# Optimization experiments

Measured on AMD Instinct MI355X. Metric: run time of the kernel, lower is better.

Reference implementation:

```python
import jax, jax.numpy as jnp
import numpy as np

N = 50000      # nodes
E = 800000     # edges
IN = 128       # in_channels
HID = 64       # hidden_channels (per head)
HEADS = 2      # GAT heads
OUT = 64       # out_channels (classes)


def segment_softmax(e, seg, num_segments):
    # softmax of per-edge scores grouped by destination node
    m = jax.ops.segment_max(e, seg, num_segments=num_segments)
    ex = jnp.exp(e - m[seg])
    s = jax.ops.segment_sum(ex, seg, num_segments=num_segments)
    return ex / s[seg]


def setup_inputs() -> dict:
    key = jax.random.key(0)
    ks = jax.random.split(key, 12)
    sc = 0.05
    return {
        "x": jax.random.normal(ks[0], (N, IN), dtype=jnp.float32),
        "edge_index": jax.random.randint(ks[1], (2, E), 0, N),
        # GATConv params: lin (no bias), att_src/att_dst, output bias
        "W1": jax.random.normal(ks[2], (IN, HEADS * HID), dtype=jnp.float32) * sc,
        "att_src": jax.random.normal(ks[3], (HEADS, HID), dtype=jnp.float32) * sc,
        "att_dst": jax.random.normal(ks[4], (HEADS, HID), dtype=jnp.float32) * sc,
        "b1": jnp.zeros((HEADS * HID,), dtype=jnp.float32),
        # TransformerConv params (heads=1): q/k/v linears + skip linear
        "Wq": jax.random.normal(ks[5], (HEADS * HID, OUT), dtype=jnp.float32) * sc,
        "bq": jnp.zeros((OUT,), dtype=jnp.float32),
        "Wk": jax.random.normal(ks[6], (HEADS * HID, OUT), dtype=jnp.float32) * sc,
        "bk": jnp.zeros((OUT,), dtype=jnp.float32),
        "Wv": jax.random.normal(ks[7], (HEADS * HID, OUT), dtype=jnp.float32) * sc,
        "bv": jnp.zeros((OUT,), dtype=jnp.float32),
        "Wskip": jax.random.normal(ks[8], (HEADS * HID, OUT), dtype=jnp.float32) * sc,
        "bskip": jnp.zeros((OUT,), dtype=jnp.float32),
    }


def reference(x, edge_index, W1, att_src, att_dst, b1,
              Wq, bq, Wk, bk, Wv, bv, Wskip, bskip):
    n = x.shape[0]
    # ---- GATConv (concat=True, add_self_loops=True, negative_slope=0.2) ----
    loops = jnp.arange(n)
    src = jnp.concatenate([edge_index[0], loops])  # message source j
    dst = jnp.concatenate([edge_index[1], loops])  # message target i
    h = (x @ W1).reshape(n, HEADS, HID)            # [N,H,C]
    a_src = (h * att_src).sum(-1)                  # [N,H]
    a_dst = (h * att_dst).sum(-1)                  # [N,H]
    e = jax.nn.leaky_relu(a_src[src] + a_dst[dst], 0.2)   # [E+N,H]
    alpha = segment_softmax(e, dst, n)                     # [E+N,H]
    out1 = jax.ops.segment_sum(alpha[..., None] * h[src], dst, num_segments=n)
    x1 = jax.nn.relu(out1.reshape(n, HEADS * HID) + b1)    # [N,H*C]
    # ---- TransformerConv (heads=1, root_weight=True, no self-loops) ----
    q = x1 @ Wq + bq
    k = x1 @ Wk + bk
    v = x1 @ Wv + bv
    s2, d2 = edge_index[0], edge_index[1]
    scores = (q[d2] * k[s2]).sum(-1) / jnp.sqrt(jnp.float32(OUT))  # [E]
    al = segment_softmax(scores, d2, n)
    agg = jax.ops.segment_sum(al[:, None] * v[s2], d2, num_segments=n)
    out = agg + x1 @ Wskip + bskip
    return jax.nn.log_softmax(out, axis=1)
```

## Files before the change

kernel.cpp:

```cpp
#include <hip/hip_runtime.h>
#include <math.h>

typedef unsigned short u16;
typedef unsigned int u32;
typedef unsigned char u8;

using bf16x8 = __attribute__((ext_vector_type(8))) short;
using f32x4  = __attribute__((ext_vector_type(4))) float;
typedef __attribute__((ext_vector_type(2))) float vf2;

__device__ __forceinline__ float lrelu02(float x){ return x > 0.f ? x : 0.2f * x; }

__device__ __forceinline__ float bf2f(u16 u){
  union { u32 i; float f; } v; v.i = ((u32)u) << 16; return v.f;
}
__device__ __forceinline__ u16 f2bf(float f){
  union { float ff; u32 i; } v; v.ff = f;
  u32 x = v.i;
  return (u16)((x + 0x7fffu + ((x >> 16) & 1u)) >> 16);
}
__device__ __forceinline__ u32 pack2(float lo, float hi){
  return (u32)f2bf(lo) | ((u32)f2bf(hi) << 16);
}
__device__ __forceinline__ u8 f2fp8(float v){
  return (u8)(__builtin_amdgcn_cvt_pk_fp8_f32(v, v, 0, false) & 0xff);
}
__device__ __forceinline__ vf2 fma2(vf2 a, vf2 b, vf2 c){
  return __builtin_elementwise_fma(a, b, c);
}

__global__ __launch_bounds__(256) void cast_x_kernel(const float* __restrict__ x,
                                                     u16* __restrict__ xbf, int total8){
  int i = blockIdx.x * 256 + threadIdx.x;
  if (i >= total8) return;
  const float4* x4 = (const float4*)x;
  float4 a = x4[(size_t)i * 2];
  float4 b = x4[(size_t)i * 2 + 1];
  uint4 w;
  w.x = pack2(a.x, a.y);
  w.y = pack2(a.z, a.w);
  w.z = pack2(b.x, b.y);
  w.w = pack2(b.z, b.w);
  ((uint4*)xbf)[i] = w;
}

__global__ __launch_bounds__(256) void cast_h_kernel(const u16* __restrict__ h2,
                                                     u8* __restrict__ h8, int total16){
  int i = blockIdx.x * 256 + threadIdx.x;
  if (i >= total16) return;
  const uint4* hp = (const uint4*)(h2 + (size_t)i * 16);
  uint4 a = hp[0], b = hp[1];
  u32 w0 = 0, w1 = 0, w2 = 0, w3 = 0;
  w0 = __builtin_amdgcn_cvt_pk_fp8_f32(bf2f((u16)(a.x & 0xffffu)), bf2f((u16)(a.x >> 16)), w0, false);
  w0 = __builtin_amdgcn_cvt_pk_fp8_f32(bf2f((u16)(a.y & 0xffffu)), bf2f((u16)(a.y >> 16)), w0, true);
  w1 = __builtin_amdgcn_cvt_pk_fp8_f32(bf2f((u16)(a.z & 0xffffu)), bf2f((u16)(a.z >> 16)), w1, false);
  w1 = __builtin_amdgcn_cvt_pk_fp8_f32(bf2f((u16)(a.w & 0xffffu)), bf2f((u16)(a.w >> 16)), w1, true);
  w2 = __builtin_amdgcn_cvt_pk_fp8_f32(bf2f((u16)(b.x & 0xffffu)), bf2f((u16)(b.x >> 16)), w2, false);
  w2 = __builtin_amdgcn_cvt_pk_fp8_f32(bf2f((u16)(b.y & 0xffffu)), bf2f((u16)(b.y >> 16)), w2, true);
  w3 = __builtin_amdgcn_cvt_pk_fp8_f32(bf2f((u16)(b.z & 0xffffu)), bf2f((u16)(b.z >> 16)), w3, false);
  w3 = __builtin_amdgcn_cvt_pk_fp8_f32(bf2f((u16)(b.w & 0xffffu)), bf2f((u16)(b.w >> 16)), w3, true);
  uint4 o = {w0, w1, w2, w3};
  ((uint4*)h8)[i] = o;
}

__global__ __launch_bounds__(256) void prep_w_kernel(const float* __restrict__ W1,
                                                     const float* __restrict__ Wq,
                                                     const float* __restrict__ Wk,
                                                     const float* __restrict__ Wv,
                                                     const float* __restrict__ Ws,
                                                     const float* __restrict__ att_src,
                                                     const float* __restrict__ att_dst,
                                                     u16* __restrict__ w1t,
                                                     u16* __restrict__ wt2,
                                                     u16* __restrict__ wxt){
  int idx = blockIdx.x * 256 + threadIdx.x;
  if (idx < 16384){
    int j = idx >> 7, k = idx & 127;
    w1t[j * 128 + k] = f2bf(W1[k * 128 + j]);
  } else if (idx < 49152){
    int i = idx - 16384;
    int mat = i >> 13;
    int r = i & 8191;
    int j = r >> 7, k = r & 127;
    const float* W = (mat == 0) ? Wq : (mat == 1) ? Wk : (mat == 2) ? Wv : Ws;
    wt2[(mat * 64 + j) * 128 + k] = f2bf(W[k * 64 + j]);
  } else if (idx < 49664){
    int i = idx - 49152;
    int j = i >> 7, k = i & 127;
    const float* av = (j & 2) ? att_dst : att_src;
    int head = j & 1;
    float s = 0.f;
#pragma unroll 8
    for (int c = 0; c < 64; c++) s += W1[k * 128 + head * 64 + c] * av[head * 64 + c];
    wxt[j * 128 + k] = f2bf(s);
  } else if (idx < 51200){
    int i = idx - 49664;
    wxt[512 + i] = 0;
  }
}

__global__ __launch_bounds__(256) void gemm1_mfma(const u16* __restrict__ xbf,
                                                  const u16* __restrict__ w1t,
                                                  const u16* __restrict__ wxt,
                                                  u16* __restrict__ h2,
                                                  float* __restrict__ asrc,
                                                  float* __restrict__ adst, int n){
  int wid = threadIdx.x >> 6, lane = threadIdx.x & 63;
  int rl = lane & 15, kh = lane >> 4;
  int br = blockIdx.x * 64 + wid * 16;
  int arow = br + rl; if (arow > n - 1) arow = n - 1;
  const u16* abase = xbf + (size_t)arow * 128 + kh * 8;
  f32x4 acc[9];
#pragma unroll
  for (int t = 0; t < 9; t++) acc[t] = (f32x4){0.f, 0.f, 0.f, 0.f};
#pragma unroll
  for (int ks = 0; ks < 4; ks++){
    bf16x8 a = *(const bf16x8*)(abase + ks * 32);
#pragma unroll
    for (int t = 0; t < 8; t++){
      bf16x8 b = *(const bf16x8*)(w1t + (size_t)(t * 16 + rl) * 128 + ks * 32 + kh * 8);
      acc[t] = __builtin_amdgcn_mfma_f32_16x16x32_bf16(a, b, acc[t], 0, 0, 0);
    }
    bf16x8 bx = *(const bf16x8*)(wxt + (size_t)rl * 128 + ks * 32 + kh * 8);
    acc[8] = __builtin_amdgcn_mfma_f32_16x16x32_bf16(a, bx, acc[8], 0, 0, 0);
  }
  int orow0 = br + kh * 4;
#pragma unroll
  for (int r = 0; r < 4; r++){
    int orow = orow0 + r;
    if (orow < n){
      u16* hp = h2 + (size_t)orow * 128 + rl;
#pragma unroll
      for (int t = 0; t < 8; t++) hp[t * 16] = f2bf(acc[t][r]);
      if (rl < 4){
        float vlv = acc[8][r];
        if (rl < 2) asrc[orow * 2 + rl] = vlv;
        else        adst[orow * 2 + (rl - 2)] = vlv;
      }
    }
  }
}

__global__ __launch_bounds__(256) void gemm2_mfma(const u16* __restrict__ x1bf,
                                                  const u16* __restrict__ wt2,
                                                  const float* __restrict__ bq,
                                                  const float* __restrict__ bk,
                                                  const float* __restrict__ bv,
                                                  const float* __restrict__ bs,
                                                  float* __restrict__ q,
                                                  u8* __restrict__ kv8,
                                                  float* __restrict__ skip, int n){
  int wid = threadIdx.x >> 6, lane = threadIdx.x & 63;
  int rl = lane & 15, kh = lane >> 4;
  int br = blockIdx.x * 64 + wid * 16;
  int arow = br + rl; if (arow > n - 1) arow = n - 1;
  const u16* abase = x1bf + (size_t)arow * 128 + kh * 8;
  f32x4 acc[16];
#pragma unroll
  for (int t = 0; t < 16; t++) acc[t] = (f32x4){0.f, 0.f, 0.f, 0.f};
#pragma unroll
  for (int ks = 0; ks < 4; ks++){
    bf16x8 a = *(const bf16x8*)(abase + ks * 32);
#pragma unroll
    for (int t = 0; t < 16; t++){
      bf16x8 b = *(const bf16x8*)(wt2 + (size_t)(t * 16 + rl) * 128 + ks * 32 + kh * 8);
      acc[t] = __builtin_amdgcn_mfma_f32_16x16x32_bf16(a, b, acc[t], 0, 0, 0);
    }
  }
  float bias_t[16];
#pragma unroll
  for (int t = 0; t < 16; t++){
    const float* bb = (t < 4) ? bq : (t < 8) ? bk : (t < 12) ? bv : bs;
    bias_t[t] = bb[(t & 3) * 16 + rl];
  }
  int orow0 = br + kh * 4;
#pragma unroll
  for (int r = 0; r < 4; r++){
    int orow = orow0 + r;
    if (orow >= n) continue;
#pragma unroll
    for (int t = 0; t < 16; t++){
      int c = (t & 3) * 16 + rl;
      float val = acc[t][r] + bias_t[t];
      if (t < 4)       q[(size_t)orow * 64 + c]    = val;
      else if (t < 8)  kv8[(size_t)orow * 128 + (c >> 3) * 16 + (c & 7)]     = f2fp8(val);
      else if (t < 12) kv8[(size_t)orow * 128 + (c >> 3) * 16 + 8 + (c & 7)] = f2fp8(val);
      else             skip[(size_t)orow * 64 + c] = val;
    }
  }
}

__global__ __launch_bounds__(256) void bucket_hist_kernel(const int* __restrict__ dst,
                                                          int* __restrict__ bc, int E){
  __shared__ int h[512];
  for (int i = threadIdx.x; i < 512; i += 256) h[i] = 0;
  __syncthreads();
  int base = blockIdx.x * 4096;
#pragma unroll
  for (int i = 0; i < 16; i++){
    int e = base + i * 256 + threadIdx.x;
    if (e < E) atomicAdd(&h[dst[e] >> 7], 1);
  }
  __syncthreads();
  for (int i = threadIdx.x; i < 512; i += 256)
    if (h[i]) atomicAdd(&bc[i], h[i]);
}

__global__ __launch_bounds__(256) void bucket_scan_kernel(const int* __restrict__ bc,
                                                          int* __restrict__ bbase,
                                                          int* __restrict__ bcur){
  __shared__ int tmp[5];
  int tid = threadIdx.x;
  int c0 = bc[2 * tid], c1 = bc[2 * tid + 1];
  int s = c0 + c1, incl = s;
  int lane = tid & 63, wid = tid >> 6;
#pragma unroll
  for (int o = 1; o < 64; o <<= 1){
    int t = __shfl_up(incl, o);
    if (lane >= o) incl += t;
  }
  if (lane == 63) tmp[wid] = incl;
  __syncthreads();
  if (tid == 0){
    int run = 0;
#pragma unroll
    for (int w2 = 0; w2 < 4; w2++){ int t = tmp[w2]; tmp[w2] = run; run += t; }
    tmp[4] = run;
  }
  __syncthreads();
  int excl = tmp[wid] + incl - s;
  bbase[2 * tid]     = excl;      bbase[2 * tid + 1] = excl + c0;
  bcur[2 * tid]      = excl;      bcur[2 * tid + 1]  = excl + c0;
  if (tid == 255) bbase[512] = tmp[4];
}

__global__ __launch_bounds__(256) void multisplit_kernel(const int* __restrict__ src,
                                                         const int* __restrict__ dst,
                                                         int* __restrict__ bcur,
                                                         uint2* __restrict__ ebuf, int E){
  __shared__ int h[512];
  __shared__ int gb[512];
  __shared__ int cur[512];
  int tid = threadIdx.x;
  for (int i = tid; i < 512; i += 256){ h[i] = 0; cur[i] = 0; }
  __syncthreads();
  int base = blockIdx.x * 4096;
  int myd[16];
#pragma unroll
  for (int i = 0; i < 16; i++){
    int e = base + i * 256 + tid;
    myd[i] = (e < E) ? dst[e] : -1;
    if (myd[i] >= 0) atomicAdd(&h[myd[i] >> 7], 1);
  }
  __syncthreads();
  for (int i = tid; i < 512; i += 256){
    int c = h[i];
    gb[i] = c ? atomicAdd(&bcur[i], c) : 0;
  }
  __syncthreads();
#pragma unroll
  for (int i = 0; i < 16; i++){
    if (myd[i] >= 0){
      int e = base + i * 256 + tid;
      int b = myd[i] >> 7;
      int r = atomicAdd(&cur[b], 1);
      uint2 ed; ed.x = (u32)src[e]; ed.y = (u32)myd[i];
      ebuf[gb[b] + r] = ed;
    }
  }
}

__global__ __launch_bounds__(256) void bucket_csr_kernel(const uint2* __restrict__ ebuf,
                                                         const int* __restrict__ bbase,
                                                         int* __restrict__ offsets,
                                                         int* __restrict__ csr,
                                                         int n, int E, int nb){
  __shared__ int deg[128];
  __shared__ int loff[128];
  __shared__ int cur[128];
  int b = blockIdx.x, tid = threadIdx.x;
  int base = bbase[b], end = bbase[b + 1];
  if (tid < 128) deg[tid] = 0;
  __syncthreads();
  for (int e = base + tid; e < end; e += 256)
    atomicAdd(&deg[ebuf[e].y & 127], 1);
  __syncthreads();
  if (tid < 64){
    int v0 = deg[2 * tid], v1 = deg[2 * tid + 1];
    int s = v0 + v1, incl = s;
#pragma unroll
    for (int o = 1; o < 64; o <<= 1){
      int t = __shfl_up(incl, o);
      if (tid >= o) incl += t;
    }
    int excl = incl - s;
    loff[2 * tid] = excl; loff[2 * tid + 1] = excl + v0;
  }
  __syncthreads();
  int node0 = b << 7;
  if (tid < 128){
    cur[tid] = loff[tid];
    int node = node0 + tid;
    if (node < n) offsets[node] = base + loff[tid];
  }
  if (b == nb - 1 && tid == 0) offsets[n] = E;
  __syncthreads();
  for (int e = base + tid; e < end; e += 256){
    uint2 ed = ebuf[e];
    int r = atomicAdd(&cur[ed.y & 127], 1);
    csr[base + r] = (int)ed.x;
  }
}

__global__ __launch_bounds__(256) void gat_agg_kernel(const u8* __restrict__ h8,
                                                      const float* __restrict__ asrc,
                                                      const float* __restrict__ adst,
                                                      const int* __restrict__ off,
                                                      const int* __restrict__ csr_src,
                                                      const float* __restrict__ b1,
                                                      u16* __restrict__ x1bf, int n){
  int node = blockIdx.x * 4 + (threadIdx.x >> 6);
  int lane = threadIdx.x & 63;
  if (node >= n) return;
  int s0 = off[node];
  int d  = off[node + 1] - s0;
  int g = lane >> 3;
  int sub = lane & 7;
  int chb = sub * 16;
  int head = sub >> 2;
  float2 ad  = ((const float2*)adst)[node];
  float2 asl = ((const float2*)asrc)[node];
  float ad_own = head ? ad.y : ad.x;
  float pself = __expf(lrelu02((head ? asl.y : asl.x) + ad_own));
  vf2 acc[8];
#pragma unroll
  for (int i = 0; i < 8; i++) acc[i] = (vf2){0.f, 0.f};
  float ps = 0.f;
#pragma unroll 2
  for (int base = 0; base < d; base += 8){
    int idx = base + g;
    bool valid = idx < d;
    int sj = csr_src[s0 + (valid ? idx : d - 1)];
    float2 as = ((const float2*)asrc)[sj];
    float p = valid ? __expf(lrelu02((head ? as.y : as.x) + ad_own)) : 0.f;
    ps += p;
    uint4 w = *(const uint4*)(h8 + (size_t)sj * 128 + chb);
    vf2 p2 = {p, p};
    acc[0] = fma2(p2, __builtin_amdgcn_cvt_pk_f32_fp8((int)w.x, false), acc[0]);
    acc[1] = fma2(p2, __builtin_amdgcn_cvt_pk_f32_fp8((int)w.x, true),  acc[1]);
    acc[2] = fma2(p2, __builtin_amdgcn_cvt_pk_f32_fp8((int)w.y, false), acc[2]);
    acc[3] = fma2(p2, __builtin_amdgcn_cvt_pk_f32_fp8((int)w.y, true),  acc[3]);
    acc[4] = fma2(p2, __builtin_amdgcn_cvt_pk_f32_fp8((int)w.z, false), acc[4]);
    acc[5] = fma2(p2, __builtin_amdgcn_cvt_pk_f32_fp8((int)w.z, true),  acc[5]);
    acc[6] = fma2(p2, __builtin_amdgcn_cvt_pk_f32_fp8((int)w.w, false), acc[6]);
    acc[7] = fma2(p2, __builtin_amdgcn_cvt_pk_f32_fp8((int)w.w, true),  acc[7]);
  }
#pragma unroll
  for (int o = 8; o <= 32; o <<= 1){
#pragma unroll
    for (int i = 0; i < 8; i++){
      acc[i][0] += __shfl_xor(acc[i][0], o);
      acc[i][1] += __shfl_xor(acc[i][1], o);
    }
    ps += __shfl_xor(ps, o);
  }
  if (lane < 8){
    float st = ps + pself;
    uint4 w = *(const uint4*)(h8 + (size_t)node * 128 + chb);
    vf2 pf2 = {pself, pself};
    acc[0] = fma2(pf2, __builtin_amdgcn_cvt_pk_f32_fp8((int)w.x, false), acc[0]);
    acc[1] = fma2(pf2, __builtin_amdgcn_cvt_pk_f32_fp8((int)w.x, true),  acc[1]);
    acc[2] = fma2(pf2, __builtin_amdgcn_cvt_pk_f32_fp8((int)w.y, false), acc[2]);
    acc[3] = fma2(pf2, __builtin_amdgcn_cvt_pk_f32_fp8((int)w.y, true),  acc[3]);
    acc[4] = fma2(pf2, __builtin_amdgcn_cvt_pk_f32_fp8((int)w.z, false), acc[4]);
    acc[5] = fma2(pf2, __builtin_amdgcn_cvt_pk_f32_fp8((int)w.z, true),  acc[5]);
    acc[6] = fma2(pf2, __builtin_amdgcn_cvt_pk_f32_fp8((int)w.w, false), acc[6]);
    acc[7] = fma2(pf2, __builtin_amdgcn_cvt_pk_f32_fp8((int)w.w, true),  acc[7]);
    const float4* bp = (const float4*)(b1 + chb);
    float4 bv0 = bp[0], bv1 = bp[1], bv2 = bp[2], bv3 = bp[3];
    float bb[16] = {bv0.x, bv0.y, bv0.z, bv0.w, bv1.x, bv1.y, bv1.z, bv1.w,
                    bv2.x, bv2.y, bv2.z, bv2.w, bv3.x, bv3.y, bv3.z, bv3.w};
    float inv = 1.f / st;
    u32 wv[8];
#pragma unroll
    for (int i = 0; i < 8; i++){
      float v0 = fmaxf(acc[i][0] * inv + bb[2*i],   0.f);
      float v1 = fmaxf(acc[i][1] * inv + bb[2*i+1], 0.f);
      wv[i] = pack2(v0, v1);
    }
    uint4 o0 = {wv[0], wv[1], wv[2], wv[3]};
    uint4 o1 = {wv[4], wv[5], wv[6], wv[7]};
    u16* xp = x1bf + (size_t)node * 128 + chb;
    *(uint4*)xp = o0;
    *(uint4*)(xp + 8) = o1;
  }
}

__global__ __launch_bounds__(256) void trans_agg_kernel(const float* __restrict__ q,
                                                        const u8* __restrict__ kv8,
                                                        const float* __restrict__ skip,
                                                        const int* __restrict__ off,
                                                        const int* __restrict__ csr_src,
                                                        float* __restrict__ out, int n){
  int node = blockIdx.x * 4 + (threadIdx.x >> 6);
  int lane = threadIdx.x & 63;
  if (node >= n) return;
  int s0 = off[node];
  int d  = off[node + 1] - s0;
  int g = lane >> 3;
  int sub = lane & 7;
  const vf2* qp = (const vf2*)(q + (size_t)node * 64 + sub * 8);
  vf2 q0 = qp[0], q1 = qp[1], q2 = qp[2], q3 = qp[3];
  vf2 acc[4];
#pragma unroll
  for (int i = 0; i < 4; i++) acc[i] = (vf2){0.f, 0.f};
  float ps = 0.f;
#pragma unroll 2
  for (int base = 0; base < d; base += 8){
    int idx = base + g;
    bool valid = idx < d;
    int sj = csr_src[s0 + (valid ? idx : d - 1)];
    uint4 w = *(const uint4*)(kv8 + (size_t)sj * 128 + sub * 16);
    vf2 d2 = {0.f, 0.f};
    d2 = fma2(q0, __builtin_amdgcn_cvt_pk_f32_fp8((int)w.x, false), d2);
    d2 = fma2(q1, __builtin_amdgcn_cvt_pk_f32_fp8((int)w.x, true),  d2);
    d2 = fma2(q2, __builtin_amdgcn_cvt_pk_f32_fp8((int)w.y, false), d2);
    d2 = fma2(q3, __builtin_amdgcn_cvt_pk_f32_fp8((int)w.y, true),  d2);
    float part = d2[0] + d2[1];
    part += __shfl_xor(part, 1);
    part += __shfl_xor(part, 2);
    part += __shfl_xor(part, 4);
    float p = valid ? __expf(part * 0.125f) : 0.f;
    ps += p;
    vf2 p2 = {p, p};
    acc[0] = fma2(p2, __builtin_amdgcn_cvt_pk_f32_fp8((int)w.z, false), acc[0]);
    acc[1] = fma2(p2, __builtin_amdgcn_cvt_pk_f32_fp8((int)w.z, true),  acc[1]);
    acc[2] = fma2(p2, __builtin_amdgcn_cvt_pk_f32_fp8((int)w.w, false), acc[2]);
    acc[3] = fma2(p2, __builtin_amdgcn_cvt_pk_f32_fp8((int)w.w, true),  acc[3]);
  }
#pragma unroll
  for (int o = 8; o <= 32; o <<= 1){
#pragma unroll
    for (int i = 0; i < 4; i++){
      acc[i][0] += __shfl_xor(acc[i][0], o);
      acc[i][1] += __shfl_xor(acc[i][1], o);
    }
    ps += __shfl_xor(ps, o);
  }
  if (lane < 8){
    const float4* sp = (const float4*)(skip + (size_t)node * 64 + sub * 8);
    float4 s0v = sp[0], s1v = sp[1];
    float sk[8] = {s0v.x, s0v.y, s0v.z, s0v.w, s1v.x, s1v.y, s1v.z, s1v.w};
    float inv = (d > 0) ? 1.f / ps : 0.f;
    float val[8];
    float mx = -3.0e38f;
#pragma unroll
    for (int i = 0; i < 8; i++){
      val[i] = sk[i] + acc[i >> 1][i & 1] * inv;
      mx = fmaxf(mx, val[i]);
    }
    mx = fmaxf(mx, __shfl_xor(mx, 1));
    mx = fmaxf(mx, __shfl_xor(mx, 2));
    mx = fmaxf(mx, __shfl_xor(mx, 4));
    float se = 0.f;
#pragma unroll
    for (int i = 0; i < 8; i++){ val[i] -= mx; se += __expf(val[i]); }
    se += __shfl_xor(se, 1);
    se += __shfl_xor(se, 2);
    se += __shfl_xor(se, 4);
    float lse = __logf(se);
    float* op = out + (size_t)node * 64 + sub * 8;
    float4 o0 = {val[0] - lse, val[1] - lse, val[2] - lse, val[3] - lse};
    float4 o4 = {val[4] - lse, val[5] - lse, val[6] - lse, val[7] - lse};
    *(float4*)(op)     = o0;
    *(float4*)(op + 4) = o4;
  }
}

extern "C" void kernel_launch(void* const* d_in, const int* in_sizes, int n_in,
                              void* d_out, int out_size, void* d_ws, size_t ws_size,
                              hipStream_t stream) {
  const float* x       = (const float*)d_in[0];
  const int*   ei      = (const int*)d_in[1];
  const float* W1      = (const float*)d_in[2];
  const float* att_src = (const float*)d_in[3];
  const float* att_dst = (const float*)d_in[4];
  const float* b1      = (const float*)d_in[5];
  const float* Wq = (const float*)d_in[6];  const float* bq = (const float*)d_in[7];
  const float* Wk = (const float*)d_in[8];  const float* bk = (const float*)d_in[9];
  const float* Wv = (const float*)d_in[10]; const float* bv = (const float*)d_in[11];
  const float* Ws = (const float*)d_in[12]; const float* bs = (const float*)d_in[13];
  float* out = (float*)d_out;

  int n = in_sizes[0] / 128;
  int E = in_sizes[1] / 2;
  const int* src = ei;
  const int* dst = ei + E;
  int nb = (n + 127) >> 7;

  char* w = (char*)d_ws;
  auto alloc = [&](size_t bytes) -> void* {
    void* p = (void*)w;
    w += (bytes + 255) & ~(size_t)255;
    return p;
  };
  u16*  xbf  = (u16*)alloc((size_t)n * 128 * 2);
  u16*  h2   = (u16*)alloc((size_t)n * 128 * 2);
  u8*   h8   = (u8*)alloc((size_t)n * 128);
  float* asrc = (float*)alloc((size_t)n * 2 * 4);
  float* adst = (float*)alloc((size_t)n * 2 * 4);
  u16*  x1bf = (u16*)alloc((size_t)n * 128 * 2);
  float* qq   = (float*)alloc((size_t)n * 64 * 4);
  u8*   kv8  = (u8*)alloc((size_t)n * 128);
  float* skip = (float*)alloc((size_t)n * 64 * 4);
  int* offsets = (int*)alloc((size_t)(n + 1) * 4);
  int* csr     = (int*)alloc((size_t)E * 4);
  int* bc      = (int*)alloc(516 * 4);
  int* bbase   = (int*)alloc(516 * 4);
  int* bcur    = (int*)alloc(516 * 4);
  u16*  w1t  = (u16*)alloc((size_t)128 * 128 * 2);
  u16*  wt2  = (u16*)alloc((size_t)256 * 128 * 2);
  u16*  wxt  = (u16*)alloc((size_t)16 * 128 * 2);
  uint2* ebuf = (uint2*)xbf;

  int eblocks = (E + 4095) / 4096;

  hipMemsetAsync(bc, 0, 513 * 4, stream);
  cast_x_kernel<<<(n * 16 + 255) / 256, 256, 0, stream>>>(x, xbf, n * 16);
  prep_w_kernel<<<200, 256, 0, stream>>>(W1, Wq, Wk, Wv, Ws, att_src, att_dst,
                                         w1t, wt2, wxt);
  gemm1_mfma<<<(n + 63) / 64, 256, 0, stream>>>(xbf, w1t, wxt, h2, asrc, adst, n);
  cast_h_kernel<<<(n * 8 + 255) / 256, 256, 0, stream>>>(h2, h8, n * 8);

  bucket_hist_kernel<<<eblocks, 256, 0, stream>>>(dst, bc, E);
  bucket_scan_kernel<<<1, 256, 0, stream>>>(bc, bbase, bcur);
  multisplit_kernel<<<eblocks, 256, 0, stream>>>(src, dst, bcur, ebuf, E);
  bucket_csr_kernel<<<nb, 256, 0, stream>>>(ebuf, bbase, offsets, csr, n, E, nb);

  gat_agg_kernel<<<(n + 3) / 4, 256, 0, stream>>>(h8, asrc, adst, offsets, csr, b1, x1bf, n);

  gemm2_mfma<<<(n + 63) / 64, 256, 0, stream>>>(x1bf, wt2, bq, bk, bv, bs,
                                                qq, kv8, skip, n);
  trans_agg_kernel<<<(n + 3) / 4, 256, 0, stream>>>(qq, kv8, skip, offsets, csr,
                                                    out, n);
}
```

Baseline: 187.3 us.

## Fuse casts into gemm1 and precompute GAT edge weights during CSR build

Drops the separate fp32→bf16 cast of x and the bf16→fp8 cast of h. gemm1 now reads fp32 x directly, converts in registers, and stages fp8 output through LDS so rows are written coalesced. The CSR build kernel now also computes the per-edge exp(leaky_relu(a_src+a_dst)) weights into a new E×float2 buffer. The GAT aggregation then reads these weights instead of gathering asrc by source index. This removes two launches and intermediate round trips, but adds an 8-byte-per-edge buffer write and read, plus a pointless ps*0.125*8 pair.

```diff
diff --git a/kernel.cpp b/kernel.cpp
--- a/kernel.cpp
+++ b/kernel.cpp
@@ -27,40 +27,6 @@
 }
 __device__ __forceinline__ vf2 fma2(vf2 a, vf2 b, vf2 c){
   return __builtin_elementwise_fma(a, b, c);
-}
-
-__global__ __launch_bounds__(256) void cast_x_kernel(const float* __restrict__ x,
-                                                     u16* __restrict__ xbf, int total8){
-  int i = blockIdx.x * 256 + threadIdx.x;
-  if (i >= total8) return;
-  const float4* x4 = (const float4*)x;
-  float4 a = x4[(size_t)i * 2];
-  float4 b = x4[(size_t)i * 2 + 1];
-  uint4 w;
-  w.x = pack2(a.x, a.y);
-  w.y = pack2(a.z, a.w);
-  w.z = pack2(b.x, b.y);
-  w.w = pack2(b.z, b.w);
-  ((uint4*)xbf)[i] = w;
-}
-
-__global__ __launch_bounds__(256) void cast_h_kernel(const u16* __restrict__ h2,
-                                                     u8* __restrict__ h8, int total16){
-  int i = blockIdx.x * 256 + threadIdx.x;
-  if (i >= total16) return;
-  const uint4* hp = (const uint4*)(h2 + (size_t)i * 16);
-  uint4 a = hp[0], b = hp[1];
-  u32 w0 = 0, w1 = 0, w2 = 0, w3 = 0;
-  w0 = __builtin_amdgcn_cvt_pk_fp8_f32(bf2f((u16)(a.x & 0xffffu)), bf2f((u16)(a.x >> 16)), w0, false);
-  w0 = __builtin_amdgcn_cvt_pk_fp8_f32(bf2f((u16)(a.y & 0xffffu)), bf2f((u16)(a.y >> 16)), w0, true);
-  w1 = __builtin_amdgcn_cvt_pk_fp8_f32(bf2f((u16)(a.z & 0xffffu)), bf2f((u16)(a.z >> 16)), w1, false);
-  w1 = __builtin_amdgcn_cvt_pk_fp8_f32(bf2f((u16)(a.w & 0xffffu)), bf2f((u16)(a.w >> 16)), w1, true);
-  w2 = __builtin_amdgcn_cvt_pk_fp8_f32(bf2f((u16)(b.x & 0xffffu)), bf2f((u16)(b.x >> 16)), w2, false);
-  w2 = __builtin_amdgcn_cvt_pk_fp8_f32(bf2f((u16)(b.y & 0xffffu)), bf2f((u16)(b.y >> 16)), w2, true);
-  w3 = __builtin_amdgcn_cvt_pk_fp8_f32(bf2f((u16)(b.z & 0xffffu)), bf2f((u16)(b.z >> 16)), w3, false);
-  w3 = __builtin_amdgcn_cvt_pk_fp8_f32(bf2f((u16)(b.w & 0xffffu)), bf2f((u16)(b.w >> 16)), w3, true);
-  uint4 o = {w0, w1, w2, w3};
-  ((uint4*)h8)[i] = o;
 }
 
 __global__ __launch_bounds__(256) void prep_w_kernel(const float* __restrict__ W1,
@@ -99,23 +65,31 @@
   }
 }
 
-__global__ __launch_bounds__(256) void gemm1_mfma(const u16* __restrict__ xbf,
+__global__ __launch_bounds__(256) void gemm1_mfma(const float* __restrict__ x,
                                                   const u16* __restrict__ w1t,
                                                   const u16* __restrict__ wxt,
-                                                  u16* __restrict__ h2,
+                                                  u8* __restrict__ h8,
                                                   float* __restrict__ asrc,
                                                   float* __restrict__ adst, int n){
+  __shared__ u8 lds8[64 * 128];
   int wid = threadIdx.x >> 6, lane = threadIdx.x & 63;
   int rl = lane & 15, kh = lane >> 4;
   int br = blockIdx.x * 64 + wid * 16;
   int arow = br + rl; if (arow > n - 1) arow = n - 1;
-  const u16* abase = xbf + (size_t)arow * 128 + kh * 8;
+  const float* ab = x + (size_t)arow * 128 + kh * 8;
   f32x4 acc[9];
 #pragma unroll
   for (int t = 0; t < 9; t++) acc[t] = (f32x4){0.f, 0.f, 0.f, 0.f};
 #pragma unroll
   for (int ks = 0; ks < 4; ks++){
-    bf16x8 a = *(const bf16x8*)(abase + ks * 32);
+    float4 xa = *(const float4*)(ab + ks * 32);
+    float4 xb = *(const float4*)(ab + ks * 32 + 4);
+    union { bf16x8 v; u32 w[4]; } au;
+    au.w[0] = pack2(xa.x, xa.y);
+    au.w[1] = pack2(xa.z, xa.w);
+    au.w[2] = pack2(xb.x, xb.y);
+    au.w[3] = pack2(xb.z, xb.w);
+    bf16x8 a = au.v;
 #pragma unroll
     for (int t = 0; t < 8; t++){
       bf16x8 b = *(const bf16x8*)(w1t + (size_t)(t * 16 + rl) * 128 + ks * 32 + kh * 8);
@@ -124,20 +98,28 @@
     bf16x8 bx = *(const bf16x8*)(wxt + (size_t)rl * 128 + ks * 32 + kh * 8);
     acc[8] = __builtin_amdgcn_mfma_f32_16x16x32_bf16(a, bx, acc[8], 0, 0, 0);
   }
-  int orow0 = br + kh * 4;
 #pragma unroll
   for (int r = 0; r < 4; r++){
-    int orow = orow0 + r;
-    if (orow < n){
-      u16* hp = h2 + (size_t)orow * 128 + rl;
-#pragma unroll
-      for (int t = 0; t < 8; t++) hp[t * 16] = f2bf(acc[t][r]);
-      if (rl < 4){
-        float vlv = acc[8][r];
-        if (rl < 2) asrc[orow * 2 + rl] = vlv;
-        else        adst[orow * 2 + (rl - 2)] = vlv;
-      }
-    }
+    int rloc = wid * 16 + kh * 4 + r;
+#pragma unroll
+    for (int t = 0; t < 8; t++)
+      lds8[rloc * 128 + t * 16 + rl] = f2fp8(acc[t][r]);
+    int orow = br + kh * 4 + r;
+    if (orow < n && rl < 4){
+      float vlv = acc[8][r];
+      if (rl < 2) asrc[orow * 2 + rl] = vlv;
+      else        adst[orow * 2 + (rl - 2)] = vlv;
+    }
+  }
+  int rrow = wid * 16 + (lane >> 2);
+  int cb = (lane & 3) * 32;
+  int grow = blockIdx.x * 64 + rrow;
+  if (grow < n){
+    uint4 v0 = *(const uint4*)&lds8[rrow * 128 + cb];
+    uint4 v1 = *(const uint4*)&lds8[rrow * 128 + cb + 16];
+    uint4* gp = (uint4*)(h8 + (size_t)grow * 128 + cb);
+    gp[0] = v0;
+    gp[1] = v1;
   }
 }
 
@@ -272,8 +254,11 @@
 
 __global__ __launch_bounds__(256) void bucket_csr_kernel(const uint2* __restrict__ ebuf,
                                                          const int* __restrict__ bbase,
+                                                         const float* __restrict__ asrc,
+                                                         const float* __restrict__ adst,
                                                          int* __restrict__ offsets,
                                                          int* __restrict__ csr,
+                                                         float2* __restrict__ pe,
                                                          int n, int E, int nb){
   __shared__ int deg[128];
   __shared__ int loff[128];
@@ -307,8 +292,16 @@
   __syncthreads();
   for (int e = base + tid; e < end; e += 256){
     uint2 ed = ebuf[e];
-    int r = atomicAdd(&cur[ed.y & 127], 1);
-    csr[base + r] = (int)ed.x;
+    int li = (int)(ed.y & 127);
+    int r = atomicAdd(&cur[li], 1);
+    int sj = (int)ed.x;
+    csr[base + r] = sj;
+    float2 as = ((const float2*)asrc)[sj];
+    float2 ad = ((const float2*)adst)[node0 + li];
+    float2 pv;
+    pv.x = __expf(lrelu02(as.x + ad.x));
+    pv.y = __expf(lrelu02(as.y + ad.y));
+    pe[base + r] = pv;
   }
 }
 
@@ -317,6 +310,7 @@
                                                       const float* __restrict__ adst,
                                                       const int* __restrict__ off,
                                                       const int* __restrict__ csr_src,
+                                                      const float2* __restrict__ pe,
                                                       const float* __restrict__ b1,
                                                       u16* __restrict__ x1bf, int n){
   int node = blockIdx.x * 4 + (threadIdx.x >> 6);
@@ -340,9 +334,10 @@
   for (int base = 0; base < d; base += 8){
     int idx = base + g;
     bool valid = idx < d;
-    int sj = csr_src[s0 + (valid ? idx : d - 1)];
-    float2 as = ((const float2*)asrc)[sj];
-    float p = valid ? __expf(lrelu02((head ? as.y : as.x) + ad_own)) : 0.f;
+    int ee = s0 + (valid ? idx : d - 1);
+    int sj = csr_src[ee];
+    float2 pv = pe[ee];
+    float p = valid ? (head ? pv.y : pv.x) : 0.f;
     ps += p;
     uint4 w = *(const uint4*)(h8 + (size_t)sj * 128 + chb);
     vf2 p2 = {p, p};
@@ -365,6 +360,8 @@
     ps += __shfl_xor(ps, o);
   }
   if (lane < 8){
+    ps *= 0.125f;
+    ps *= 8.f;
     float st = ps + pself;
     uint4 w = *(const uint4*)(h8 + (size_t)node * 128 + chb);
     vf2 pf2 = {pself, pself};
@@ -504,8 +501,6 @@
     w += (bytes + 255) & ~(size_t)255;
     return p;
   };
-  u16*  xbf  = (u16*)alloc((size_t)n * 128 * 2);
-  u16*  h2   = (u16*)alloc((size_t)n * 128 * 2);
   u8*   h8   = (u8*)alloc((size_t)n * 128);
   float* asrc = (float*)alloc((size_t)n * 2 * 4);
   float* adst = (float*)alloc((size_t)n * 2 * 4);
@@ -515,29 +510,30 @@
   float* skip = (float*)alloc((size_t)n * 64 * 4);
   int* offsets = (int*)alloc((size_t)(n + 1) * 4);
   int* csr     = (int*)alloc((size_t)E * 4);
+  float2* pe   = (float2*)alloc((size_t)E * 8);
   int* bc      = (int*)alloc(516 * 4);
   int* bbase   = (int*)alloc(516 * 4);
   int* bcur    = (int*)alloc(516 * 4);
   u16*  w1t  = (u16*)alloc((size_t)128 * 128 * 2);
   u16*  wt2  = (u16*)alloc((size_t)256 * 128 * 2);
   u16*  wxt  = (u16*)alloc((size_t)16 * 128 * 2);
-  uint2* ebuf = (uint2*)xbf;
+  uint2* ebuf = (uint2*)x1bf;
 
   int eblocks = (E + 4095) / 4096;
 
   hipMemsetAsync(bc, 0, 513 * 4, stream);
-  cast_x_kernel<<<(n * 16 + 255) / 256, 256, 0, stream>>>(x, xbf, n * 16);
   prep_w_kernel<<<200, 256, 0, stream>>>(W1, Wq, Wk, Wv, Ws, att_src, att_dst,
                                          w1t, wt2, wxt);
-  gemm1_mfma<<<(n + 63) / 64, 256, 0, stream>>>(xbf, w1t, wxt, h2, asrc, adst, n);
-  cast_h_kernel<<<(n * 8 + 255) / 256, 256, 0, stream>>>(h2, h8, n * 8);
+  gemm1_mfma<<<(n + 63) / 64, 256, 0, stream>>>(x, w1t, wxt, h8, asrc, adst, n);
 
   bucket_hist_kernel<<<eblocks, 256, 0, stream>>>(dst, bc, E);
   bucket_scan_kernel<<<1, 256, 0, stream>>>(bc, bbase, bcur);
   multisplit_kernel<<<eblocks, 256, 0, stream>>>(src, dst, bcur, ebuf, E);
-  bucket_csr_kernel<<<nb, 256, 0, stream>>>(ebuf, bbase, offsets, csr, n, E, nb);
-
-  gat_agg_kernel<<<(n + 3) / 4, 256, 0, stream>>>(h8, asrc, adst, offsets, csr, b1, x1bf, n);
+  bucket_csr_kernel<<<nb, 256, 0, stream>>>(ebuf, bbase, asrc, adst,
+                                            offsets, csr, pe, n, E, nb);
+
+  gat_agg_kernel<<<(n + 3) / 4, 256, 0, stream>>>(h8, asrc, adst, offsets, csr, pe,
+                                                  b1, x1bf, n);
 
   gemm2_mfma<<<(n + 63) / 64, 256, 0, stream>>>(x1bf, wt2, bq, bk, bv, bs,
                                                 qq, kv8, skip, n);
```

Measured after the change: 180.0 us. 3.9% less time.
